# Performance work log

Measured on AMD Instinct MI355X. Metric: run time of the kernel, lower is better.

Reference implementation:

```python
import jax, jax.numpy as jnp
import numpy as np

ZETA = 1.1
GAMMA = -0.1

B, F, D = 1024, 32, 128


def setup_inputs() -> dict:
    key = jax.random.key(0)
    k1, k2 = jax.random.split(key)
    feature = jax.random.normal(k1, (B, F, D), dtype=jnp.float32)
    # nn.Parameter init: normal(mean=0, std=0.001)
    matrix = jax.random.normal(k2, (F, F, D, D), dtype=jnp.float32) * 0.001
    return {"feature": feature, "matrix": matrix}


def reference(feature, matrix):
    # feature: [B, F, D]; matrix (logAlpha of hard-concrete gate): [F, F, D, D]
    nF = matrix.shape[0]
    # strict upper-triangular pair mask over (i, j)
    mask = jnp.triu(jnp.ones((nF, nF), dtype=feature.dtype), k=1)
    # deterministic (eval-mode) hard-concrete gate: stretch + clamp
    s = jax.nn.sigmoid(matrix)
    z = jnp.clip(s * (ZETA - GAMMA) + GAMMA, 0.0, 1.0)
    l0_out = mask[:, :, None, None] * z  # [F, F, D, D]
    # out[b,i,j] = f_i^T Z_ij f_j  == sum_{d,e} f[b,i,d] * Z[i,j,d,e] * f[b,j,e]
    # (faithful to: (f[:, :, None, :, None] @ f[:, None, :, None, :]) * Z, summed over (d, e))
    out = jnp.einsum('bid,ijde,bje->bij', feature, l0_out, feature)
    return out
```

## Files before the change

kernel.cpp:

```cpp
#include <hip/hip_runtime.h>

#define B_SZ 1024
#define F_SZ 32
#define D_SZ 128
#define FD   (F_SZ * D_SZ)
#define NPAIR 496

typedef __bf16 bf16x8 __attribute__((ext_vector_type(8)));
typedef float floatx4 __attribute__((ext_vector_type(4)));
typedef unsigned short u16x4 __attribute__((ext_vector_type(4)));
typedef unsigned short u16x8 __attribute__((ext_vector_type(8)));

__device__ __forceinline__ unsigned short f2bf(float f) {
  unsigned u = __float_as_uint(f);
  u += 0x7fffu + ((u >> 16) & 1u);
  return (unsigned short)(u >> 16);
}

__device__ __forceinline__ void gload_lds16(const void* g, void* l) {
  __builtin_amdgcn_global_load_lds(
      (const __attribute__((address_space(1))) unsigned int*)g,
      (__attribute__((address_space(3))) unsigned int*)l,
      16, 0, 0);
}

__global__ void feat_cvt_kernel(const float* __restrict__ feat,
                                unsigned short* __restrict__ featB) {
  const int idx8 = blockIdx.x * 256 + threadIdx.x;
  const float4* f4 = (const float4*)feat;
  const float4 v0 = f4[(size_t)idx8 * 2];
  const float4 v1 = f4[(size_t)idx8 * 2 + 1];
  u16x8 h;
  h[0] = f2bf(v0.x); h[1] = f2bf(v0.y); h[2] = f2bf(v0.z); h[3] = f2bf(v0.w);
  h[4] = f2bf(v1.x); h[5] = f2bf(v1.y); h[6] = f2bf(v1.z); h[7] = f2bf(v1.w);
  *(u16x8*)&featB[(size_t)idx8 * 8] = h;
}

__global__ void z_prep_kernel(const float* __restrict__ mat,
                              unsigned short* __restrict__ ZT) {
  __shared__ unsigned short tr[128 * 132];
  const int t = threadIdx.x;

  int p = blockIdx.x, i = 0;
  while (p >= F_SZ - 1 - i) { p -= F_SZ - 1 - i; ++i; }
  const int j = i + 1 + p;

  const float* zp = mat + (((size_t)i * F_SZ + j) * (size_t)(D_SZ * D_SZ));
  #pragma unroll 4
  for (int it = 0; it < 16; ++it) {
    int idx4 = it * 256 + t;
    int d = idx4 >> 5, e4 = (idx4 & 31) * 4;
    const float4 v = *(const float4*)(zp + d * D_SZ + e4);
    float zs[4] = {v.x, v.y, v.z, v.w};
    #pragma unroll
    for (int c = 0; c < 4; ++c) {
      float s = 1.0f / (1.0f + __expf(-zs[c]));
      float z = fminf(1.0f, fmaxf(0.0f, fmaf(s, 1.2f, -0.1f)));
      tr[(e4 + c) * 132 + d] = f2bf(z);
    }
  }
  __syncthreads();

  unsigned short* zo = ZT + (size_t)blockIdx.x * (D_SZ * D_SZ);
  #pragma unroll 2
  for (int it = 0; it < 8; ++it) {
    int G = it * 256 + t;
    int e = G >> 4, gp = G & 15;
    int g = gp ^ (e & 7);
    u16x4 lo = *(const u16x4*)&tr[e * 132 + g * 8];
    u16x4 hi = *(const u16x4*)&tr[e * 132 + g * 8 + 4];
    *(u16x4*)&zo[e * 128 + gp * 8]     = lo;
    *(u16x4*)&zo[e * 128 + gp * 8 + 4] = hi;
  }
}

__global__ __launch_bounds__(256, 2)
void interaction_pair_kernel(const float* __restrict__ feat,
                             const unsigned short* __restrict__ featB,
                             const unsigned short* __restrict__ ZT,
                             float* __restrict__ out) {
  __shared__ unsigned short sZ[128 * 128];

  const int t    = threadIdx.x;
  const int w    = t >> 6;
  const int lane = t & 63;
  const int l15  = lane & 15;
  const int quad = lane >> 4;

  const int pid   = blockIdx.x >> 2;
  const int split = blockIdx.x & 3;
  int p = pid, i = 0;
  while (p >= F_SZ - 1 - i) { p -= F_SZ - 1 - i; ++i; }
  const int j = i + 1 + p;

  {
    const char* src = (const char*)(ZT + (size_t)pid * (D_SZ * D_SZ));
    #pragma unroll
    for (int it = 0; it < 8; ++it) {
      int off = it * 4096 + w * 1024;
      gload_lds16(src + off + lane * 16, (char*)sZ + off);
    }
  }
  __syncthreads();

  bf16x8 zfr[4][8];
  #pragma unroll
  for (int k0 = 0; k0 < 4; ++k0)
    #pragma unroll
    for (int nf = 0; nf < 8; ++nf) {
      const int e    = nf * 16 + l15;
      const int dcol = k0 * 32 + quad * 8;
      const int soff = e * 128 + (dcol ^ ((e & 7) << 3));
      zfr[k0][nf] = *(const bf16x8*)&sZ[soff];
    }

  const int b0 = split * 256;
  for (int bt = 0; bt < 2; ++bt) {
    const int rowbase = b0 + bt * 128 + w * 32;

    floatx4 acc[2][8];
    #pragma unroll
    for (int mf = 0; mf < 2; ++mf)
      #pragma unroll
      for (int nf = 0; nf < 8; ++nf)
        acc[mf][nf] = (floatx4){0.f, 0.f, 0.f, 0.f};

    #pragma unroll
    for (int mf = 0; mf < 2; ++mf) {
      bf16x8 af[4];
      const unsigned short* ap =
          featB + (size_t)(rowbase + mf * 16 + l15) * FD + i * D_SZ + quad * 8;
      #pragma unroll
      for (int k0 = 0; k0 < 4; ++k0) af[k0] = *(const bf16x8*)(ap + k0 * 32);
      #pragma unroll
      for (int k0 = 0; k0 < 4; ++k0)
        #pragma unroll
        for (int nf = 0; nf < 8; ++nf)
          acc[mf][nf] = __builtin_amdgcn_mfma_f32_16x16x32_bf16(
              af[k0], zfr[k0][nf], acc[mf][nf], 0, 0, 0);
    }

    #pragma unroll
    for (int mf = 0; mf < 2; ++mf) {
      float pl[4] = {0.f, 0.f, 0.f, 0.f};
      const int rb = rowbase + mf * 16 + quad * 4;
      #pragma unroll
      for (int nf = 0; nf < 8; ++nf) {
        const int col = nf * 16 + l15;
        const float* fj = feat + (size_t)rb * FD + j * D_SZ + col;
        floatx4 c = acc[mf][nf];
        pl[0] += c[0] * fj[0];
        pl[1] += c[1] * fj[FD];
        pl[2] += c[2] * fj[2 * FD];
        pl[3] += c[3] * fj[3 * FD];
      }
      #pragma unroll
      for (int off = 1; off < 16; off <<= 1) {
        pl[0] += __shfl_xor(pl[0], off, 64);
        pl[1] += __shfl_xor(pl[1], off, 64);
        pl[2] += __shfl_xor(pl[2], off, 64);
        pl[3] += __shfl_xor(pl[3], off, 64);
      }
      if (l15 == 0) {
        size_t ob = (size_t)rb * (F_SZ * F_SZ) + (size_t)i * F_SZ + j;
        out[ob]                   = pl[0];
        out[ob + 1 * F_SZ * F_SZ] = pl[1];
        out[ob + 2 * F_SZ * F_SZ] = pl[2];
        out[ob + 3 * F_SZ * F_SZ] = pl[3];
      }
    }
  }
}

extern "C" void kernel_launch(void* const* d_in, const int* in_sizes, int n_in,
                              void* d_out, int out_size, void* d_ws, size_t ws_size,
                              hipStream_t stream) {
  const float* feat = (const float*)d_in[0];
  const float* mat  = (const float*)d_in[1];
  float* out = (float*)d_out;

  unsigned short* featB = (unsigned short*)d_ws;
  unsigned short* ZT    = featB + (size_t)B_SZ * F_SZ * D_SZ;

  hipMemsetAsync(out, 0, (size_t)out_size * sizeof(float), stream);

  feat_cvt_kernel<<<dim3((B_SZ * F_SZ * D_SZ) / (256 * 8)), dim3(256), 0, stream>>>(feat, featB);
  z_prep_kernel<<<dim3(NPAIR), dim3(256), 0, stream>>>(mat, ZT);
  interaction_pair_kernel<<<dim3(NPAIR * 4), dim3(256), 0, stream>>>(feat, featB, ZT, out);
}
```

Baseline: 155.4 us.

## Fuse prep kernels and compute second contraction with MFMA via hi/lo bf16 split

Merges the feature conversion, Z preparation and output zeroing into one prep kernel, replacing the memset and two launches. Feature data is split into hi and lo bf16 parts so the second contraction with f_j can run as MFMA. The intermediate product is staged in LDS as bf16, replacing the fp32 scalar dot products and shuffle reductions. The grid is split eight ways per pair and the occupancy hint is raised to three blocks. Z fragments are now read from LDS inside the loop instead of being held in registers. The extra featLo buffer adds memory traffic, and rounding the intermediate to bf16 may cost accuracy.

```diff
diff --git a/kernel.cpp b/kernel.cpp
--- a/kernel.cpp
+++ b/kernel.cpp
@@ -7,14 +7,18 @@
 #define NPAIR 496
 
 typedef __bf16 bf16x8 __attribute__((ext_vector_type(8)));
+typedef __bf16 bf16x4 __attribute__((ext_vector_type(4)));
 typedef float floatx4 __attribute__((ext_vector_type(4)));
-typedef unsigned short u16x4 __attribute__((ext_vector_type(4)));
 typedef unsigned short u16x8 __attribute__((ext_vector_type(8)));
 
 __device__ __forceinline__ unsigned short f2bf(float f) {
   unsigned u = __float_as_uint(f);
   u += 0x7fffu + ((u >> 16) & 1u);
   return (unsigned short)(u >> 16);
+}
+
+__device__ __forceinline__ float bf2f(unsigned short h) {
+  return __uint_as_float(((unsigned)h) << 16);
 }
 
 __device__ __forceinline__ void gload_lds16(const void* g, void* l) {
@@ -24,71 +28,83 @@
       16, 0, 0);
 }
 
-__global__ void feat_cvt_kernel(const float* __restrict__ feat,
-                                unsigned short* __restrict__ featB) {
-  const int idx8 = blockIdx.x * 256 + threadIdx.x;
-  const float4* f4 = (const float4*)feat;
-  const float4 v0 = f4[(size_t)idx8 * 2];
-  const float4 v1 = f4[(size_t)idx8 * 2 + 1];
-  u16x8 h;
-  h[0] = f2bf(v0.x); h[1] = f2bf(v0.y); h[2] = f2bf(v0.z); h[3] = f2bf(v0.w);
-  h[4] = f2bf(v1.x); h[5] = f2bf(v1.y); h[6] = f2bf(v1.z); h[7] = f2bf(v1.w);
-  *(u16x8*)&featB[(size_t)idx8 * 8] = h;
-}
+__global__ __launch_bounds__(256)
+void prep_kernel(const float* __restrict__ feat, const float* __restrict__ mat,
+                 unsigned short* __restrict__ featHi, unsigned short* __restrict__ featLo,
+                 unsigned short* __restrict__ ZT, float* __restrict__ out) {
+  const int bid = blockIdx.x, t = threadIdx.x;
+  __shared__ unsigned short tr[128 * 72];
 
-__global__ void z_prep_kernel(const float* __restrict__ mat,
-                              unsigned short* __restrict__ ZT) {
-  __shared__ unsigned short tr[128 * 132];
-  const int t = threadIdx.x;
-
-  int p = blockIdx.x, i = 0;
-  while (p >= F_SZ - 1 - i) { p -= F_SZ - 1 - i; ++i; }
-  const int j = i + 1 + p;
-
-  const float* zp = mat + (((size_t)i * F_SZ + j) * (size_t)(D_SZ * D_SZ));
-  #pragma unroll 4
-  for (int it = 0; it < 16; ++it) {
-    int idx4 = it * 256 + t;
-    int d = idx4 >> 5, e4 = (idx4 & 31) * 4;
-    const float4 v = *(const float4*)(zp + d * D_SZ + e4);
-    float zs[4] = {v.x, v.y, v.z, v.w};
+  if (bid < 2 * NPAIR) {
+    const int pid = bid >> 1, h = bid & 1, d0 = h * 64;
+    int p = pid, i = 0;
+    while (p >= F_SZ - 1 - i) { p -= F_SZ - 1 - i; ++i; }
+    const int j = i + 1 + p;
+    const float* zp = mat + (((size_t)i * F_SZ + j) * (size_t)(D_SZ * D_SZ));
     #pragma unroll
-    for (int c = 0; c < 4; ++c) {
-      float s = 1.0f / (1.0f + __expf(-zs[c]));
-      float z = fminf(1.0f, fmaxf(0.0f, fmaf(s, 1.2f, -0.1f)));
-      tr[(e4 + c) * 132 + d] = f2bf(z);
+    for (int it = 0; it < 8; ++it) {
+      int idx4 = it * 256 + t;
+      int dl = idx4 >> 5, e4 = (idx4 & 31) * 4;
+      const float4 v = *(const float4*)(zp + (size_t)(d0 + dl) * D_SZ + e4);
+      float zs[4] = {v.x, v.y, v.z, v.w};
+      #pragma unroll
+      for (int c = 0; c < 4; ++c) {
+        float s = 1.0f / (1.0f + __expf(-zs[c]));
+        float z = fminf(1.0f, fmaxf(0.0f, fmaf(s, 1.2f, -0.1f)));
+        tr[(e4 + c) * 72 + dl] = f2bf(z);
+      }
     }
-  }
-  __syncthreads();
-
-  unsigned short* zo = ZT + (size_t)blockIdx.x * (D_SZ * D_SZ);
-  #pragma unroll 2
-  for (int it = 0; it < 8; ++it) {
-    int G = it * 256 + t;
-    int e = G >> 4, gp = G & 15;
-    int g = gp ^ (e & 7);
-    u16x4 lo = *(const u16x4*)&tr[e * 132 + g * 8];
-    u16x4 hi = *(const u16x4*)&tr[e * 132 + g * 8 + 4];
-    *(u16x4*)&zo[e * 128 + gp * 8]     = lo;
-    *(u16x4*)&zo[e * 128 + gp * 8 + 4] = hi;
+    __syncthreads();
+    #pragma unroll
+    for (int it = 0; it < 4; ++it) {
+      int G = it * 256 + t;
+      int e = G >> 3, gl = G & 7;
+      int gs = gl ^ (e & 7);
+      u16x8 v = *(const u16x8*)&tr[e * 72 + gs * 8];
+      *(u16x8*)&ZT[(size_t)pid * (D_SZ * D_SZ) + e * 128 + d0 + gl * 8] = v;
+    }
+  } else if (bid < 2 * NPAIR + 1024) {
+    int idx = (bid - 2 * NPAIR) * 256 + t;
+    const float4* f4 = (const float4*)feat + (size_t)idx * 4;
+    #pragma unroll
+    for (int q = 0; q < 2; ++q) {
+      float4 a = f4[q * 2], b = f4[q * 2 + 1];
+      float vs[8] = {a.x, a.y, a.z, a.w, b.x, b.y, b.z, b.w};
+      u16x8 hi, lo;
+      #pragma unroll
+      for (int c = 0; c < 8; ++c) {
+        unsigned short hh = f2bf(vs[c]);
+        hi[c] = hh;
+        lo[c] = f2bf(vs[c] - bf2f(hh));
+      }
+      *(u16x8*)&featHi[(size_t)idx * 16 + q * 8] = hi;
+      *(u16x8*)&featLo[(size_t)idx * 16 + q * 8] = lo;
+    }
+  } else {
+    int idx = (bid - (2 * NPAIR + 1024)) * 256 + t;
+    float4* o4 = (float4*)out + (size_t)idx * 4;
+    float4 z = {0.f, 0.f, 0.f, 0.f};
+    o4[0] = z; o4[1] = z; o4[2] = z; o4[3] = z;
   }
 }
 
-__global__ __launch_bounds__(256, 2)
-void interaction_pair_kernel(const float* __restrict__ feat,
-                             const unsigned short* __restrict__ featB,
+__global__ __launch_bounds__(256, 3)
+void interaction_pair_kernel(const unsigned short* __restrict__ featHi,
+                             const unsigned short* __restrict__ featLo,
                              const unsigned short* __restrict__ ZT,
                              float* __restrict__ out) {
   __shared__ unsigned short sZ[128 * 128];
+  __shared__ unsigned short sW[4 * 2048];
 
   const int t    = threadIdx.x;
   const int w    = t >> 6;
   const int lane = t & 63;
   const int l15  = lane & 15;
   const int quad = lane >> 4;
+  const int swz  = (l15 & 7) << 4;
 
-  const int pid   = blockIdx.x >> 2;
-  const int split = blockIdx.x & 3;
+  const int pid   = blockIdx.x >> 3;
+  const int split = blockIdx.x & 7;
   int p = pid, i = 0;
   while (p >= F_SZ - 1 - i) { p -= F_SZ - 1 - i; ++i; }
   const int j = i + 1 + p;
@@ -103,71 +119,55 @@
   }
   __syncthreads();
 
-  bf16x8 zfr[4][8];
+  const int rbase = split * 128 + w * 32;
+
+  floatx4 acc[8][2];
   #pragma unroll
-  for (int k0 = 0; k0 < 4; ++k0)
+  for (int m = 0; m < 8; ++m) {
+    acc[m][0] = (floatx4){0.f, 0.f, 0.f, 0.f};
+    acc[m][1] = (floatx4){0.f, 0.f, 0.f, 0.f};
+  }
+
+  #pragma unroll
+  for (int k0 = 0; k0 < 4; ++k0) {
+    const int dq = k0 * 32 + quad * 8;
+    bf16x8 b0f = *(const bf16x8*)&featHi[(size_t)(rbase +      l15) * FD + i * D_SZ + dq];
+    bf16x8 b1f = *(const bf16x8*)&featHi[(size_t)(rbase + 16 + l15) * FD + i * D_SZ + dq];
     #pragma unroll
-    for (int nf = 0; nf < 8; ++nf) {
-      const int e    = nf * 16 + l15;
-      const int dcol = k0 * 32 + quad * 8;
-      const int soff = e * 128 + (dcol ^ ((e & 7) << 3));
-      zfr[k0][nf] = *(const bf16x8*)&sZ[soff];
+    for (int m = 0; m < 8; ++m) {
+      const int e = m * 16 + l15;
+      bf16x8 za = *(const bf16x8*)((const char*)sZ + e * 256 + ((2 * dq) ^ swz));
+      acc[m][0] = __builtin_amdgcn_mfma_f32_16x16x32_bf16(za, b0f, acc[m][0], 0, 0, 0);
+      acc[m][1] = __builtin_amdgcn_mfma_f32_16x16x32_bf16(za, b1f, acc[m][1], 0, 0, 0);
     }
+  }
 
-  const int b0 = split * 256;
-  for (int bt = 0; bt < 2; ++bt) {
-    const int rowbase = b0 + bt * 128 + w * 32;
-
-    floatx4 acc[2][8];
+  char* wb = (char*)(sW + w * 2048);
+  #pragma unroll
+  for (int n = 0; n < 2; ++n) {
     #pragma unroll
-    for (int mf = 0; mf < 2; ++mf)
-      #pragma unroll
-      for (int nf = 0; nf < 8; ++nf)
-        acc[mf][nf] = (floatx4){0.f, 0.f, 0.f, 0.f};
-
+    for (int m = 0; m < 8; ++m) {
+      floatx4 c = acc[m][n];
+      bf16x4 v = {(__bf16)c[0], (__bf16)c[1], (__bf16)c[2], (__bf16)c[3]};
+      const int e0 = m * 16 + quad * 4;
+      *(bf16x4*)(wb + l15 * 256 + ((2 * e0) ^ swz)) = v;
+    }
+    const int row = rbase + n * 16 + l15;
+    const unsigned short* fj_h = featHi + (size_t)row * FD + j * D_SZ;
+    const unsigned short* fj_l = featLo + (size_t)row * FD + j * D_SZ;
+    floatx4 g = (floatx4){0.f, 0.f, 0.f, 0.f};
     #pragma unroll
-    for (int mf = 0; mf < 2; ++mf) {
-      bf16x8 af[4];
-      const unsigned short* ap =
-          featB + (size_t)(rowbase + mf * 16 + l15) * FD + i * D_SZ + quad * 8;
-      #pragma unroll
-      for (int k0 = 0; k0 < 4; ++k0) af[k0] = *(const bf16x8*)(ap + k0 * 32);
-      #pragma unroll
-      for (int k0 = 0; k0 < 4; ++k0)
-        #pragma unroll
-        for (int nf = 0; nf < 8; ++nf)
-          acc[mf][nf] = __builtin_amdgcn_mfma_f32_16x16x32_bf16(
-              af[k0], zfr[k0][nf], acc[mf][nf], 0, 0, 0);
+    for (int k0 = 0; k0 < 4; ++k0) {
+      bf16x8 wf = *(const bf16x8*)(wb + l15 * 256 + ((k0 * 64 + quad * 16) ^ swz));
+      bf16x8 ah = *(const bf16x8*)(fj_h + k0 * 32 + quad * 8);
+      bf16x8 al = *(const bf16x8*)(fj_l + k0 * 32 + quad * 8);
+      g = __builtin_amdgcn_mfma_f32_16x16x32_bf16(ah, wf, g, 0, 0, 0);
+      g = __builtin_amdgcn_mfma_f32_16x16x32_bf16(al, wf, g, 0, 0, 0);
     }
-
-    #pragma unroll
-    for (int mf = 0; mf < 2; ++mf) {
-      float pl[4] = {0.f, 0.f, 0.f, 0.f};
-      const int rb = rowbase + mf * 16 + quad * 4;
-      #pragma unroll
-      for (int nf = 0; nf < 8; ++nf) {
-        const int col = nf * 16 + l15;
-        const float* fj = feat + (size_t)rb * FD + j * D_SZ + col;
-        floatx4 c = acc[mf][nf];
-        pl[0] += c[0] * fj[0];
-        pl[1] += c[1] * fj[FD];
-        pl[2] += c[2] * fj[2 * FD];
-        pl[3] += c[3] * fj[3 * FD];
-      }
-      #pragma unroll
-      for (int off = 1; off < 16; off <<= 1) {
-        pl[0] += __shfl_xor(pl[0], off, 64);
-        pl[1] += __shfl_xor(pl[1], off, 64);
-        pl[2] += __shfl_xor(pl[2], off, 64);
-        pl[3] += __shfl_xor(pl[3], off, 64);
-      }
-      if (l15 == 0) {
-        size_t ob = (size_t)rb * (F_SZ * F_SZ) + (size_t)i * F_SZ + j;
-        out[ob]                   = pl[0];
-        out[ob + 1 * F_SZ * F_SZ] = pl[1];
-        out[ob + 2 * F_SZ * F_SZ] = pl[2];
-        out[ob + 3 * F_SZ * F_SZ] = pl[3];
-      }
+    if ((l15 >> 2) == quad) {
+      const int r = l15 & 3;
+      float val = g[r];
+      out[(size_t)row * (F_SZ * F_SZ) + (size_t)i * F_SZ + j] = val;
     }
   }
 }
@@ -179,12 +179,11 @@
   const float* mat  = (const float*)d_in[1];
   float* out = (float*)d_out;
 
-  unsigned short* featB = (unsigned short*)d_ws;
-  unsigned short* ZT    = featB + (size_t)B_SZ * F_SZ * D_SZ;
+  unsigned short* featHi = (unsigned short*)d_ws;
+  unsigned short* featLo = featHi + (size_t)B_SZ * F_SZ * D_SZ;
+  unsigned short* ZT     = featLo + (size_t)B_SZ * F_SZ * D_SZ;
 
-  hipMemsetAsync(out, 0, (size_t)out_size * sizeof(float), stream);
-
-  feat_cvt_kernel<<<dim3((B_SZ * F_SZ * D_SZ) / (256 * 8)), dim3(256), 0, stream>>>(feat, featB);
-  z_prep_kernel<<<dim3(NPAIR), dim3(256), 0, stream>>>(mat, ZT);
-  interaction_pair_kernel<<<dim3(NPAIR * 4), dim3(256), 0, stream>>>(feat, featB, ZT, out);
+  const int prep_grid = 2 * NPAIR + 1024 + 256;
+  prep_kernel<<<dim3(prep_grid), dim3(256), 0, stream>>>(feat, mat, featHi, featLo, ZT, out);
+  interaction_pair_kernel<<<dim3(NPAIR * 8), dim3(256), 0, stream>>>(featHi, featLo, ZT, out);
 }
```

Result: no change. 158.1 us (+1.7%).
